# Kernel optimization log

Measured on AMD Instinct MI355X. Metric: run time of the kernel, lower is better.

Reference implementation:

```python
import jax, jax.numpy as jnp
import numpy as np

HID = 512
EMB = 768
TOP_K = 8
LN_EPS = 1e-5
NORM_EPS = 1e-12


def _mlp_ln(x, W1, b1, W2, b2, g, beta):
    # Linear -> ReLU -> Linear -> LayerNorm
    h = jax.nn.relu(x @ W1 + b1)
    h = h @ W2 + b2
    mu = jnp.mean(h, axis=-1, keepdims=True)
    var = jnp.var(h, axis=-1, keepdims=True)
    return (h - mu) * jax.lax.rsqrt(var + LN_EPS) * g + beta


def _l2norm(x):
    n = jnp.linalg.norm(x, axis=-1, keepdims=True)
    return x / jnp.maximum(n, NORM_EPS)


def setup_inputs() -> dict:
    key = jax.random.key(0)
    ks = jax.random.split(key, 12)
    s_in = 1.0 / np.sqrt(EMB)
    s_h = 1.0 / np.sqrt(HID)
    inp = {
        "query_embeddings": jax.random.normal(ks[0], (64, 32, EMB), jnp.float32),
        "doc_embeddings": jax.random.normal(ks[1], (50000, 16, EMB), jnp.float32),
        "qW1": jax.random.normal(ks[2], (EMB, HID), jnp.float32) * s_in,
        "qb1": jnp.zeros((HID,), jnp.float32),
        "qW2": jax.random.normal(ks[3], (HID, HID), jnp.float32) * s_h,
        "qb2": jnp.zeros((HID,), jnp.float32),
        "qg": jnp.ones((HID,), jnp.float32),
        "qbeta": jnp.zeros((HID,), jnp.float32),
        "dW1": jax.random.normal(ks[4], (EMB, HID), jnp.float32) * s_in,
        "db1": jnp.zeros((HID,), jnp.float32),
        "dW2": jax.random.normal(ks[5], (HID, HID), jnp.float32) * s_h,
        "db2": jnp.zeros((HID,), jnp.float32),
        "dg": jnp.ones((HID,), jnp.float32),
        "dbeta": jnp.zeros((HID,), jnp.float32),
        "pW": jax.random.normal(ks[6], (HID, HID), jnp.float32) * s_h,
        "pb": jnp.zeros((HID,), jnp.float32),
        "temperature": jnp.asarray(1.0, jnp.float32),
    }
    return inp


def reference(query_embeddings, doc_embeddings, qW1, qb1, qW2, qb2, qg, qbeta,
              dW1, db1, dW2, db2, dg, dbeta, pW, pb, temperature):
    # Mean-pool over token dims, encode with MLP+LayerNorm
    q_repr = _mlp_ln(query_embeddings.mean(axis=1), qW1, qb1, qW2, qb2, qg, qbeta)  # [B,H]
    d_repr = _mlp_ln(doc_embeddings.mean(axis=1), dW1, db1, dW2, db2, dg, dbeta)    # [N,H]
    q_norm = _l2norm(q_repr @ pW + pb)
    d_norm = _l2norm(d_repr @ pW + pb)
    scores = (q_norm @ d_norm.T) / temperature  # [B,N]
    top_k_scores, top_k_indices = jax.lax.top_k(scores, TOP_K)  # [B,K]
    retrieved_docs = doc_embeddings[top_k_indices]  # [B,K,doc_len,EMB]
    return top_k_scores, retrieved_docs
```

## Files before the change

kernel.cpp:

```cpp
#include <hip/hip_runtime.h>

#define NQ 64
#define ND 50000
#define QTOK 32
#define DTOK 16
#define EMB 768
#define HID 512

typedef short s16x8 __attribute__((ext_vector_type(8)));
typedef float f32x4 __attribute__((ext_vector_type(4)));

__device__ __forceinline__ unsigned short f2bf(float f) {
    union { float f; unsigned u; } x; x.f = f;
    unsigned r = x.u + 0x7fffu + ((x.u >> 16) & 1u);
    return (unsigned short)(r >> 16);
}
__device__ __forceinline__ float bf2f(unsigned short h) {
    union { unsigned u; float f; } x; x.u = ((unsigned)h) << 16;
    return x.f;
}
__device__ __forceinline__ void pack2A(float va, float vb, unsigned& w0, unsigned& w1, unsigned& w2) {
    unsigned ha = f2bf(va); unsigned la = f2bf(va - bf2f((unsigned short)ha));
    unsigned hb = f2bf(vb); unsigned lb = f2bf(vb - bf2f((unsigned short)hb));
    w0 = ha | (la << 16);
    w1 = ha | (hb << 16);
    w2 = lb | (hb << 16);
}
__device__ __forceinline__ void pack2B(float va, float vb, unsigned& w0, unsigned& w1, unsigned& w2) {
    unsigned ha = f2bf(va); unsigned la = f2bf(va - bf2f((unsigned short)ha));
    unsigned hb = f2bf(vb); unsigned lb = f2bf(vb - bf2f((unsigned short)hb));
    w0 = ha | (ha << 16);
    w1 = la | (hb << 16);
    w2 = hb | (lb << 16);
}

__device__ __forceinline__ void gload_lds16(const void* g, void* l) {
    __builtin_amdgcn_global_load_lds(
        (const __attribute__((address_space(1))) void*)g,
        (__attribute__((address_space(3))) void*)l, 16, 0, 0);
}

__global__ void pool_kernel(const float* __restrict__ in, float* __restrict__ out, int T) {
    int r = blockIdx.x;
    int t = threadIdx.x;
    const float4* ip = (const float4*)in + (size_t)r * T * (EMB / 4);
    float4 acc = make_float4(0.f, 0.f, 0.f, 0.f);
    for (int i = 0; i < T; ++i) {
        float4 v = ip[(size_t)i * (EMB / 4) + t];
        acc.x += v.x; acc.y += v.y; acc.z += v.z; acc.w += v.w;
    }
    float s = 1.0f / (float)T;
    acc.x *= s; acc.y *= s; acc.z *= s; acc.w *= s;
    ((float4*)out)[(size_t)r * (EMB / 4) + t] = acc;
}

__global__ void pool_aug(const float* __restrict__ in, ushort* __restrict__ out) {
    int r = blockIdx.x, t = threadIdx.x;
    const float4* ip = (const float4*)in + (size_t)r * DTOK * (EMB / 4) + t;
    float4 a = make_float4(0.f, 0.f, 0.f, 0.f);
    #pragma unroll
    for (int i = 0; i < DTOK; ++i) {
        float4 v = ip[(size_t)i * (EMB / 4)];
        a.x += v.x; a.y += v.y; a.z += v.z; a.w += v.w;
    }
    const float s = 1.0f / (float)DTOK;
    unsigned w0, w1, w2, w3, w4, w5;
    pack2A(a.x * s, a.y * s, w0, w1, w2);
    pack2A(a.z * s, a.w * s, w3, w4, w5);
    uint2* q = (uint2*)(out + (size_t)r * (3 * EMB) + t * 12);
    q[0] = make_uint2(w0, w1); q[1] = make_uint2(w2, w3); q[2] = make_uint2(w4, w5);
}

__global__ void wconv(const float* __restrict__ W, ushort* __restrict__ Wp, int K) {
    int n = blockIdx.x;
    for (int k = threadIdx.x; k < K; k += blockDim.x) {
        float v = W[(size_t)k * HID + n];
        unsigned short hi = f2bf(v);
        unsigned short lo = f2bf(v - bf2f(hi));
        ushort* p = Wp + (size_t)n * 3 * K + 3 * k;
        p[0] = hi; p[1] = hi; p[2] = lo;
    }
}

template <int MODE>
__global__ __launch_bounds__(512) void mfma_gemm2(const ushort* __restrict__ A,
                                                  const ushort* __restrict__ B,
                                                  const float* __restrict__ bias,
                                                  void* __restrict__ out,
                                                  int M, int N_B, int K2, long ldo,
                                                  const float* __restrict__ temp) {
    __shared__ ushort As[128 * 64];
    __shared__ ushort Bs[256 * 64];
    const int bm = blockIdx.x * 128;
    const int bn = blockIdx.y * 256;
    const int tid = threadIdx.x;
    const int lane = tid & 63;
    const int wave = tid >> 6;
    const int wr = wave >> 2;
    const int wc = wave & 3;
    f32x4 acc[4][4] = {};

    for (int k0 = 0; k0 < K2; k0 += 64) {
        #pragma unroll
        for (int c = 0; c < 2; ++c) {
            int row = c * 64 + (tid >> 3);
            int s   = tid & 7;
            int grow = bm + row; if (grow >= M) grow = M - 1;
            int ks = (s ^ (row & 7)) << 3;
            gload_lds16(A + (size_t)grow * K2 + k0 + ks, As + row * 64 + s * 8);
        }
        #pragma unroll
        for (int c = 0; c < 4; ++c) {
            int n = c * 64 + (tid >> 3);
            int s = tid & 7;
            int gn = bn + n; if (gn >= N_B) gn = N_B - 1;
            int ks = (s ^ (n & 7)) << 3;
            gload_lds16(B + (size_t)gn * K2 + k0 + ks, Bs + n * 64 + s * 8);
        }
        __syncthreads();

        #pragma unroll
        for (int kk = 0; kk < 2; ++kk) {
            const int sp = kk * 4 + (lane >> 4);
            s16x8 a[4], b[4];
            #pragma unroll
            for (int i = 0; i < 4; ++i) {
                int r = wr * 64 + i * 16 + (lane & 15);
                a[i] = *(const s16x8*)(As + r * 64 + ((sp ^ (r & 7)) << 3));
            }
            #pragma unroll
            for (int j = 0; j < 4; ++j) {
                int n = wc * 64 + j * 16 + (lane & 15);
                b[j] = *(const s16x8*)(Bs + n * 64 + ((sp ^ (n & 7)) << 3));
            }
            #pragma unroll
            for (int i = 0; i < 4; ++i)
                #pragma unroll
                for (int j = 0; j < 4; ++j)
                    acc[i][j] = __builtin_amdgcn_mfma_f32_16x16x32_bf16(a[i], b[j], acc[i][j], 0, 0, 0);
        }
        __syncthreads();
    }

    float scale = (MODE == 2) ? (1.0f / temp[0]) : 0.0f;
    #pragma unroll
    for (int j = 0; j < 4; ++j) {
        int col = bn + wc * 64 + j * 16 + (lane & 15);
        float bv = (MODE == 2) ? 0.0f : bias[col];
        #pragma unroll
        for (int i = 0; i < 4; ++i) {
            #pragma unroll
            for (int r = 0; r < 4; ++r) {
                int grow = bm + wr * 64 + i * 16 + ((lane >> 4) << 2) + r;
                if (grow >= M) continue;
                float v = acc[i][j][r];
                if (MODE == 0) {
                    ((float*)out)[(size_t)grow * HID + col] = v + bv;
                } else if (MODE == 1) {
                    v = fmaxf(v + bv, 0.0f);
                    unsigned short hi = f2bf(v);
                    unsigned short lo = f2bf(v - bf2f(hi));
                    ushort* op = (ushort*)out + (size_t)grow * (3 * HID) + 3 * col;
                    op[0] = hi; op[1] = lo; op[2] = hi;
                } else {
                    if (col < N_B) ((float*)out)[(size_t)grow * ldo + col] = v * scale;
                }
            }
        }
    }
}

__global__ __launch_bounds__(256) void ln_kernel(float* __restrict__ x,
                                                 const float* __restrict__ g,
                                                 const float* __restrict__ be, int M) {
    int wv = threadIdx.x >> 6, lane = threadIdx.x & 63;
    int row = blockIdx.x * 4 + wv;
    if (row >= M) return;
    float4* p = (float4*)(x + (size_t)row * HID);
    float4 a = p[lane * 2], b = p[lane * 2 + 1];
    float s  = a.x + a.y + a.z + a.w + b.x + b.y + b.z + b.w;
    float sq = a.x*a.x + a.y*a.y + a.z*a.z + a.w*a.w
             + b.x*b.x + b.y*b.y + b.z*b.z + b.w*b.w;
    #pragma unroll
    for (int o = 32; o > 0; o >>= 1) { s += __shfl_xor(s, o); sq += __shfl_xor(sq, o); }
    float mu  = s * (1.0f / HID);
    float var = sq * (1.0f / HID) - mu * mu;
    float r   = rsqrtf(var + 1e-5f);
    const float4* gp = (const float4*)g;
    const float4* bp = (const float4*)be;
    float4 g0 = gp[lane * 2], g1 = gp[lane * 2 + 1];
    float4 b0 = bp[lane * 2], b1 = bp[lane * 2 + 1];
    a.x = (a.x - mu) * r * g0.x + b0.x;  a.y = (a.y - mu) * r * g0.y + b0.y;
    a.z = (a.z - mu) * r * g0.z + b0.z;  a.w = (a.w - mu) * r * g0.w + b0.w;
    b.x = (b.x - mu) * r * g1.x + b1.x;  b.y = (b.y - mu) * r * g1.y + b1.y;
    b.z = (b.z - mu) * r * g1.z + b1.z;  b.w = (b.w - mu) * r * g1.w + b1.w;
    p[lane * 2] = a; p[lane * 2 + 1] = b;
}

__global__ __launch_bounds__(256) void ln_aug(const float* __restrict__ x,
                                              const float* __restrict__ g,
                                              const float* __restrict__ be,
                                              ushort* __restrict__ out, int M) {
    int wv = threadIdx.x >> 6, lane = threadIdx.x & 63;
    int row = blockIdx.x * 4 + wv;
    if (row >= M) return;
    const float4* p = (const float4*)(x + (size_t)row * HID);
    float4 a = p[lane * 2], b = p[lane * 2 + 1];
    float s  = a.x + a.y + a.z + a.w + b.x + b.y + b.z + b.w;
    float sq = a.x*a.x + a.y*a.y + a.z*a.z + a.w*a.w
             + b.x*b.x + b.y*b.y + b.z*b.z + b.w*b.w;
    #pragma unroll
    for (int o = 32; o > 0; o >>= 1) { s += __shfl_xor(s, o); sq += __shfl_xor(sq, o); }
    float mu  = s * (1.0f / HID);
    float var = sq * (1.0f / HID) - mu * mu;
    float r   = rsqrtf(var + 1e-5f);
    const float4* gp = (const float4*)g;
    const float4* bp = (const float4*)be;
    float4 g0 = gp[lane * 2], g1 = gp[lane * 2 + 1];
    float4 b0 = bp[lane * 2], b1 = bp[lane * 2 + 1];
    float v0 = (a.x - mu) * r * g0.x + b0.x, v1 = (a.y - mu) * r * g0.y + b0.y;
    float v2 = (a.z - mu) * r * g0.z + b0.z, v3 = (a.w - mu) * r * g0.w + b0.w;
    float v4 = (b.x - mu) * r * g1.x + b1.x, v5 = (b.y - mu) * r * g1.y + b1.y;
    float v6 = (b.z - mu) * r * g1.z + b1.z, v7 = (b.w - mu) * r * g1.w + b1.w;
    unsigned w[12];
    pack2A(v0, v1, w[0], w[1], w[2]);
    pack2A(v2, v3, w[3], w[4], w[5]);
    pack2A(v4, v5, w[6], w[7], w[8]);
    pack2A(v6, v7, w[9], w[10], w[11]);
    uint4* q = (uint4*)(out + (size_t)row * (3 * HID) + lane * 24);
    q[0] = make_uint4(w[0], w[1], w[2], w[3]);
    q[1] = make_uint4(w[4], w[5], w[6], w[7]);
    q[2] = make_uint4(w[8], w[9], w[10], w[11]);
}

__global__ __launch_bounds__(256) void l2_augB(const float* __restrict__ x,
                                               ushort* __restrict__ out, int M) {
    int wv = threadIdx.x >> 6, lane = threadIdx.x & 63;
    int row = blockIdx.x * 4 + wv;
    if (row >= M) return;
    const float4* p = (const float4*)(x + (size_t)row * HID);
    float4 a = p[lane * 2], b = p[lane * 2 + 1];
    float sq = a.x*a.x + a.y*a.y + a.z*a.z + a.w*a.w
             + b.x*b.x + b.y*b.y + b.z*b.z + b.w*b.w;
    #pragma unroll
    for (int o = 32; o > 0; o >>= 1) sq += __shfl_xor(sq, o);
    float n = sqrtf(sq);
    float r = 1.0f / fmaxf(n, 1e-12f);
    float v0 = a.x*r, v1 = a.y*r, v2 = a.z*r, v3 = a.w*r;
    float v4 = b.x*r, v5 = b.y*r, v6 = b.z*r, v7 = b.w*r;
    unsigned w[12];
    pack2B(v0, v1, w[0], w[1], w[2]);
    pack2B(v2, v3, w[3], w[4], w[5]);
    pack2B(v4, v5, w[6], w[7], w[8]);
    pack2B(v6, v7, w[9], w[10], w[11]);
    uint4* q = (uint4*)(out + (size_t)row * (3 * HID) + lane * 24);
    q[0] = make_uint4(w[0], w[1], w[2], w[3]);
    q[1] = make_uint4(w[4], w[5], w[6], w[7]);
    q[2] = make_uint4(w[8], w[9], w[10], w[11]);
}

__global__ __launch_bounds__(256) void l2_kernel(float* __restrict__ x, int M) {
    int wv = threadIdx.x >> 6, lane = threadIdx.x & 63;
    int row = blockIdx.x * 4 + wv;
    if (row >= M) return;
    float4* p = (float4*)(x + (size_t)row * HID);
    float4 a = p[lane * 2], b = p[lane * 2 + 1];
    float sq = a.x*a.x + a.y*a.y + a.z*a.z + a.w*a.w
             + b.x*b.x + b.y*b.y + b.z*b.z + b.w*b.w;
    #pragma unroll
    for (int o = 32; o > 0; o >>= 1) sq += __shfl_xor(sq, o);
    float n = sqrtf(sq);
    float r = 1.0f / fmaxf(n, 1e-12f);
    a.x *= r; a.y *= r; a.z *= r; a.w *= r;
    b.x *= r; b.y *= r; b.z *= r; b.w *= r;
    p[lane * 2] = a; p[lane * 2 + 1] = b;
}

__global__ __launch_bounds__(256) void fp32_augA(const float* __restrict__ x,
                                                 ushort* __restrict__ out, int M) {
    int wv = threadIdx.x >> 6, lane = threadIdx.x & 63;
    int row = blockIdx.x * 4 + wv;
    if (row >= M) return;
    const float4* p = (const float4*)(x + (size_t)row * HID);
    float4 a = p[lane * 2], b = p[lane * 2 + 1];
    unsigned w[12];
    pack2A(a.x, a.y, w[0], w[1], w[2]);
    pack2A(a.z, a.w, w[3], w[4], w[5]);
    pack2A(b.x, b.y, w[6], w[7], w[8]);
    pack2A(b.z, b.w, w[9], w[10], w[11]);
    uint4* q = (uint4*)(out + (size_t)row * (3 * HID) + lane * 24);
    q[0] = make_uint4(w[0], w[1], w[2], w[3]);
    q[1] = make_uint4(w[4], w[5], w[6], w[7]);
    q[2] = make_uint4(w[8], w[9], w[10], w[11]);
}

template <int RELU>
__global__ __launch_bounds__(256) void gemm_nn(const float* __restrict__ A,
                                               const float* __restrict__ W,
                                               const float* __restrict__ bias,
                                               float* __restrict__ C,
                                               int M, int K, int N) {
    __shared__ float As[16][68];
    __shared__ float Bs[16][64];
    const int bm = blockIdx.x * 64;
    const int bn = blockIdx.y * 64;
    const int tid = threadIdx.x;
    const int tx = tid & 15, ty = tid >> 4;
    float acc[4][4] = {};
    for (int k0 = 0; k0 < K; k0 += 16) {
        {
            int row = tid >> 2;
            int kk  = (tid & 3) << 2;
            int gr  = bm + row;
            float4 v = make_float4(0.f, 0.f, 0.f, 0.f);
            if (gr < M) v = *(const float4*)(A + (size_t)gr * K + k0 + kk);
            As[kk + 0][row] = v.x; As[kk + 1][row] = v.y;
            As[kk + 2][row] = v.z; As[kk + 3][row] = v.w;
        }
        {
            int n  = tid & 63;
            int kb = tid >> 6;
            #pragma unroll
            for (int q = 0; q < 4; ++q) {
                int kr = kb + q * 4;
                Bs[kr][n] = W[(size_t)(k0 + kr) * N + bn + n];
            }
        }
        __syncthreads();
        #pragma unroll
        for (int k = 0; k < 16; ++k) {
            float4 av = *(const float4*)&As[k][ty << 2];
            float4 bv = *(const float4*)&Bs[k][tx << 2];
            float a[4] = {av.x, av.y, av.z, av.w};
            float b[4] = {bv.x, bv.y, bv.z, bv.w};
            #pragma unroll
            for (int i = 0; i < 4; ++i)
                #pragma unroll
                for (int j = 0; j < 4; ++j)
                    acc[i][j] = fmaf(a[i], b[j], acc[i][j]);
        }
        __syncthreads();
    }
    #pragma unroll
    for (int i = 0; i < 4; ++i) {
        int gr = bm + (ty << 2) + i;
        if (gr >= M) continue;
        #pragma unroll
        for (int j = 0; j < 4; ++j) {
            int gc = bn + (tx << 2) + j;
            float v = acc[i][j] + bias[gc];
            if (RELU) v = fmaxf(v, 0.0f);
            C[(size_t)gr * N + gc] = v;
        }
    }
}

__global__ __launch_bounds__(256) void topk_kernel(const float* __restrict__ scores,
                                                   float* __restrict__ out_scores,
                                                   int* __restrict__ out_idx, int N) {
    __shared__ float ls[2048];
    __shared__ int   li[2048];
    const int q   = blockIdx.x;
    const int tid = threadIdx.x;
    const float* row = scores + (size_t)q * N;
    float s[8]; int ix[8];
    #pragma unroll
    for (int i = 0; i < 8; ++i) { s[i] = -1e30f; ix[i] = 0x7fffffff; }
    for (int j = tid; j < N; j += 256) {
        float v = row[j];
        if (v > s[7]) {
            s[7] = v; ix[7] = j;
            #pragma unroll
            for (int t = 7; t > 0; --t) {
                bool sw = (s[t] > s[t-1]) || (s[t] == s[t-1] && ix[t] < ix[t-1]);
                if (sw) {
                    float tv = s[t]; s[t] = s[t-1]; s[t-1] = tv;
                    int   ti = ix[t]; ix[t] = ix[t-1]; ix[t-1] = ti;
                }
            }
        }
    }
    #pragma unroll
    for (int i = 0; i < 8; ++i) { ls[tid * 8 + i] = s[i]; li[tid * 8 + i] = ix[i]; }
    __syncthreads();
    for (int w = 64; w >= 1; w >>= 2) {
        if (tid < w) {
            #pragma unroll
            for (int i = 0; i < 8; ++i) { s[i] = -1e30f; ix[i] = 0x7fffffff; }
            #pragma unroll
            for (int c = 0; c < 32; ++c) {
                float v  = ls[tid * 32 + c];
                int   vi = li[tid * 32 + c];
                bool better = (v > s[7]) || (v == s[7] && vi < ix[7]);
                if (better) {
                    s[7] = v; ix[7] = vi;
                    #pragma unroll
                    for (int t = 7; t > 0; --t) {
                        bool sw = (s[t] > s[t-1]) || (s[t] == s[t-1] && ix[t] < ix[t-1]);
                        if (sw) {
                            float tv = s[t]; s[t] = s[t-1]; s[t-1] = tv;
                            int   ti = ix[t]; ix[t] = ix[t-1]; ix[t-1] = ti;
                        }
                    }
                }
            }
        }
        __syncthreads();
        if (tid < w) {
            #pragma unroll
            for (int i = 0; i < 8; ++i) { ls[tid * 8 + i] = s[i]; li[tid * 8 + i] = ix[i]; }
        }
        __syncthreads();
    }
    if (tid < 8) {
        out_scores[(size_t)q * 8 + tid] = ls[tid];
        out_idx[q * 8 + tid]            = li[tid];
    }
}

__global__ __launch_bounds__(256) void gather_kernel(const float* __restrict__ docs,
                                                     const int* __restrict__ idx,
                                                     float* __restrict__ out) {
    const int b = blockIdx.x;
    const int d = idx[b];
    const float4* src = (const float4*)(docs + (size_t)d * DTOK * EMB);
    float4*       dst = (float4*)(out + (size_t)b * DTOK * EMB);
    for (int i = threadIdx.x; i < DTOK * EMB / 4; i += 256) dst[i] = src[i];
}

extern "C" void kernel_launch(void* const* d_in, const int* in_sizes, int n_in,
                              void* d_out, int out_size, void* d_ws, size_t ws_size,
                              hipStream_t stream) {
    const float* qe   = (const float*)d_in[0];
    const float* de   = (const float*)d_in[1];
    const float* qW1  = (const float*)d_in[2];
    const float* qb1  = (const float*)d_in[3];
    const float* qW2  = (const float*)d_in[4];
    const float* qb2  = (const float*)d_in[5];
    const float* qg   = (const float*)d_in[6];
    const float* qbe  = (const float*)d_in[7];
    const float* dW1  = (const float*)d_in[8];
    const float* db1  = (const float*)d_in[9];
    const float* dW2  = (const float*)d_in[10];
    const float* db2  = (const float*)d_in[11];
    const float* dg   = (const float*)d_in[12];
    const float* dbe  = (const float*)d_in[13];
    const float* pW   = (const float*)d_in[14];
    const float* pb   = (const float*)d_in[15];
    const float* temp = (const float*)d_in[16];

    float* out = (float*)d_out;

    char* w = (char*)d_ws;
    float*  scores = (float*)w;                 w += (size_t)NQ * ND * 4;
    ushort* W1p    = (ushort*)w;                w += (size_t)HID * 3 * EMB * 2;
    ushort* W2p    = (ushort*)w;                w += (size_t)HID * 3 * HID * 2;
    ushort* pWp    = (ushort*)w;                w += (size_t)HID * 3 * HID * 2;
    float*  qpool  = (float*)w;                 w += (size_t)NQ * EMB * 4;
    float*  qh1    = (float*)w;                 w += (size_t)NQ * HID * 4;
    float*  qh2    = (float*)w;                 w += (size_t)NQ * HID * 4;
    float*  qn     = (float*)w;                 w += (size_t)NQ * HID * 4;
    ushort* qaug   = (ushort*)w;                w += (size_t)NQ * 3 * HID * 2;
    int*    tidx   = (int*)w;                   w += 4096;
    ushort* pooled = (ushort*)w;                w += (size_t)ND * 3 * EMB * 2;
    ushort* h1a    = (ushort*)w;                w += (size_t)ND * 3 * HID * 2;
    float*  h2     = (float*)w;                 w += (size_t)ND * HID * 4;
    ushort* lna    = pooled;
    float*  pproj  = h2;
    ushort* Daug   = h1a;

    const int GM = (ND + 127) / 128;

    wconv<<<HID, 256, 0, stream>>>(dW1, W1p, EMB);
    wconv<<<HID, 256, 0, stream>>>(dW2, W2p, HID);
    wconv<<<HID, 256, 0, stream>>>(pW,  pWp, HID);

    pool_kernel<<<NQ, 192, 0, stream>>>(qe, qpool, QTOK);
    gemm_nn<1><<<dim3(1, 8), 256, 0, stream>>>(qpool, qW1, qb1, qh1, NQ, EMB, HID);
    gemm_nn<0><<<dim3(1, 8), 256, 0, stream>>>(qh1, qW2, qb2, qh2, NQ, HID, HID);
    ln_kernel<<<(NQ + 3) / 4, 256, 0, stream>>>(qh2, qg, qbe, NQ);
    gemm_nn<0><<<dim3(1, 8), 256, 0, stream>>>(qh2, pW, pb, qn, NQ, HID, HID);
    l2_kernel<<<(NQ + 3) / 4, 256, 0, stream>>>(qn, NQ);
    fp32_augA<<<(NQ + 3) / 4, 256, 0, stream>>>(qn, qaug, NQ);

    pool_aug<<<ND, 192, 0, stream>>>(de, pooled);
    mfma_gemm2<1><<<dim3(GM, 2), 512, 0, stream>>>(pooled, W1p, db1, h1a, ND, HID, 3 * EMB, 0, nullptr);
    mfma_gemm2<0><<<dim3(GM, 2), 512, 0, stream>>>(h1a, W2p, db2, h2, ND, HID, 3 * HID, 0, nullptr);
    ln_aug<<<(ND + 3) / 4, 256, 0, stream>>>(h2, dg, dbe, lna, ND);
    mfma_gemm2<0><<<dim3(GM, 2), 512, 0, stream>>>(lna, pWp, pb, pproj, ND, HID, 3 * HID, 0, nullptr);
    l2_augB<<<(ND + 3) / 4, 256, 0, stream>>>(pproj, Daug, ND);

    mfma_gemm2<2><<<dim3(1, (ND + 255) / 256), 512, 0, stream>>>(qaug, Daug, nullptr, scores,
                                                                 NQ, ND, 3 * HID, (long)ND, temp);

    topk_kernel<<<NQ, 256, 0, stream>>>(scores, out, tidx, ND);
    gather_kernel<<<NQ * 8, 256, 0, stream>>>(de, tidx, out + NQ * 8);
}
```

Measured before the change: 1.563 ms.

## Fuse LayerNorm and L2 norm into full-row GEMM epilogues, unify query path

Result: slower. 1.594 ms (+2.0%).

```diff
diff --git a/kernel.cpp b/kernel.cpp
--- a/kernel.cpp
+++ b/kernel.cpp
@@ -19,6 +19,16 @@
     union { unsigned u; float f; } x; x.u = ((unsigned)h) << 16;
     return x.f;
 }
+__device__ __forceinline__ void packA1(float v, ushort* p) {
+    unsigned short hi = f2bf(v);
+    unsigned short lo = f2bf(v - bf2f(hi));
+    p[0] = hi; p[1] = lo; p[2] = hi;
+}
+__device__ __forceinline__ void packB1(float v, ushort* p) {
+    unsigned short hi = f2bf(v);
+    unsigned short lo = f2bf(v - bf2f(hi));
+    p[0] = hi; p[1] = hi; p[2] = lo;
+}
 __device__ __forceinline__ void pack2A(float va, float vb, unsigned& w0, unsigned& w1, unsigned& w2) {
     unsigned ha = f2bf(va); unsigned la = f2bf(va - bf2f((unsigned short)ha));
     unsigned hb = f2bf(vb); unsigned lb = f2bf(vb - bf2f((unsigned short)hb));
@@ -26,13 +36,6 @@
     w1 = ha | (hb << 16);
     w2 = lb | (hb << 16);
 }
-__device__ __forceinline__ void pack2B(float va, float vb, unsigned& w0, unsigned& w1, unsigned& w2) {
-    unsigned ha = f2bf(va); unsigned la = f2bf(va - bf2f((unsigned short)ha));
-    unsigned hb = f2bf(vb); unsigned lb = f2bf(vb - bf2f((unsigned short)hb));
-    w0 = ha | (ha << 16);
-    w1 = la | (hb << 16);
-    w2 = hb | (lb << 16);
-}
 
 __device__ __forceinline__ void gload_lds16(const void* g, void* l) {
     __builtin_amdgcn_global_load_lds(
@@ -40,30 +43,15 @@
         (__attribute__((address_space(3))) void*)l, 16, 0, 0);
 }
 
-__global__ void pool_kernel(const float* __restrict__ in, float* __restrict__ out, int T) {
-    int r = blockIdx.x;
-    int t = threadIdx.x;
-    const float4* ip = (const float4*)in + (size_t)r * T * (EMB / 4);
-    float4 acc = make_float4(0.f, 0.f, 0.f, 0.f);
+__global__ void pool_aug(const float* __restrict__ in, ushort* __restrict__ out, int T) {
+    int r = blockIdx.x, t = threadIdx.x;
+    const float4* ip = (const float4*)in + (size_t)r * T * (EMB / 4) + t;
+    float4 a = make_float4(0.f, 0.f, 0.f, 0.f);
     for (int i = 0; i < T; ++i) {
-        float4 v = ip[(size_t)i * (EMB / 4) + t];
-        acc.x += v.x; acc.y += v.y; acc.z += v.z; acc.w += v.w;
-    }
-    float s = 1.0f / (float)T;
-    acc.x *= s; acc.y *= s; acc.z *= s; acc.w *= s;
-    ((float4*)out)[(size_t)r * (EMB / 4) + t] = acc;
-}
-
-__global__ void pool_aug(const float* __restrict__ in, ushort* __restrict__ out) {
-    int r = blockIdx.x, t = threadIdx.x;
-    const float4* ip = (const float4*)in + (size_t)r * DTOK * (EMB / 4) + t;
-    float4 a = make_float4(0.f, 0.f, 0.f, 0.f);
-    #pragma unroll
-    for (int i = 0; i < DTOK; ++i) {
         float4 v = ip[(size_t)i * (EMB / 4)];
         a.x += v.x; a.y += v.y; a.z += v.z; a.w += v.w;
     }
-    const float s = 1.0f / (float)DTOK;
+    const float s = 1.0f / (float)T;
     unsigned w0, w1, w2, w3, w4, w5;
     pack2A(a.x * s, a.y * s, w0, w1, w2);
     pack2A(a.z * s, a.w * s, w3, w4, w5);
@@ -75,47 +63,49 @@
     int n = blockIdx.x;
     for (int k = threadIdx.x; k < K; k += blockDim.x) {
         float v = W[(size_t)k * HID + n];
-        unsigned short hi = f2bf(v);
-        unsigned short lo = f2bf(v - bf2f(hi));
         ushort* p = Wp + (size_t)n * 3 * K + 3 * k;
-        p[0] = hi; p[1] = hi; p[2] = lo;
-    }
-}
-
-template <int MODE>
-__global__ __launch_bounds__(512) void mfma_gemm2(const ushort* __restrict__ A,
-                                                  const ushort* __restrict__ B,
-                                                  const float* __restrict__ bias,
-                                                  void* __restrict__ out,
-                                                  int M, int N_B, int K2, long ldo,
-                                                  const float* __restrict__ temp) {
-    __shared__ ushort As[128 * 64];
-    __shared__ ushort Bs[256 * 64];
-    const int bm = blockIdx.x * 128;
-    const int bn = blockIdx.y * 256;
+        packB1(v, p);
+    }
+}
+
+template <int EPI, int NW>
+__global__ __launch_bounds__(NW * 64) void gemmF(const ushort* __restrict__ A,
+                                                 const ushort* __restrict__ B,
+                                                 const float* __restrict__ bias,
+                                                 const float* __restrict__ gamma,
+                                                 const float* __restrict__ beta,
+                                                 void* __restrict__ out,
+                                                 int M, int N_B, int K2, long ldo,
+                                                 const float* __restrict__ temp) {
+    constexpr int BN = NW * 64;
+    constexpr int NTHR = NW * 64;
+    __shared__ ushort As[64 * 64];
+    __shared__ ushort Bs[BN * 64];
+    __shared__ float red[2][NW][64];
+    __shared__ float mu_s[64], rs_s[64];
+    const int bm = blockIdx.x * 64;
+    const int bn = blockIdx.y * BN;
     const int tid = threadIdx.x;
     const int lane = tid & 63;
-    const int wave = tid >> 6;
-    const int wr = wave >> 2;
-    const int wc = wave & 3;
+    const int wc = tid >> 6;
     f32x4 acc[4][4] = {};
 
     for (int k0 = 0; k0 < K2; k0 += 64) {
         #pragma unroll
-        for (int c = 0; c < 2; ++c) {
-            int row = c * 64 + (tid >> 3);
-            int s   = tid & 7;
-            int grow = bm + row; if (grow >= M) grow = M - 1;
+        for (int c = 0; c < 512 / NTHR; ++c) {
+            int idx = c * NTHR + tid;
+            int row = idx >> 3, s = idx & 7;
+            int gr = bm + row; if (gr >= M) gr = M - 1;
             int ks = (s ^ (row & 7)) << 3;
-            gload_lds16(A + (size_t)grow * K2 + k0 + ks, As + row * 64 + s * 8);
-        }
-        #pragma unroll
-        for (int c = 0; c < 4; ++c) {
-            int n = c * 64 + (tid >> 3);
-            int s = tid & 7;
+            gload_lds16(A + (size_t)gr * K2 + k0 + ks, As + idx * 8);
+        }
+        #pragma unroll
+        for (int c = 0; c < 8; ++c) {
+            int idx = c * NTHR + tid;
+            int n = idx >> 3, s = idx & 7;
             int gn = bn + n; if (gn >= N_B) gn = N_B - 1;
             int ks = (s ^ (n & 7)) << 3;
-            gload_lds16(B + (size_t)gn * K2 + k0 + ks, Bs + n * 64 + s * 8);
+            gload_lds16(B + (size_t)gn * K2 + k0 + ks, Bs + idx * 8);
         }
         __syncthreads();
 
@@ -125,7 +115,7 @@
             s16x8 a[4], b[4];
             #pragma unroll
             for (int i = 0; i < 4; ++i) {
-                int r = wr * 64 + i * 16 + (lane & 15);
+                int r = i * 16 + (lane & 15);
                 a[i] = *(const s16x8*)(As + r * 64 + ((sp ^ (r & 7)) << 3));
             }
             #pragma unroll
@@ -142,217 +132,94 @@
         __syncthreads();
     }
 
-    float scale = (MODE == 2) ? (1.0f / temp[0]) : 0.0f;
-    #pragma unroll
-    for (int j = 0; j < 4; ++j) {
-        int col = bn + wc * 64 + j * 16 + (lane & 15);
-        float bv = (MODE == 2) ? 0.0f : bias[col];
-        #pragma unroll
-        for (int i = 0; i < 4; ++i) {
-            #pragma unroll
-            for (int r = 0; r < 4; ++r) {
-                int grow = bm + wr * 64 + i * 16 + ((lane >> 4) << 2) + r;
-                if (grow >= M) continue;
-                float v = acc[i][j][r];
-                if (MODE == 0) {
-                    ((float*)out)[(size_t)grow * HID + col] = v + bv;
-                } else if (MODE == 1) {
-                    v = fmaxf(v + bv, 0.0f);
-                    unsigned short hi = f2bf(v);
-                    unsigned short lo = f2bf(v - bf2f(hi));
-                    ushort* op = (ushort*)out + (size_t)grow * (3 * HID) + 3 * col;
-                    op[0] = hi; op[1] = lo; op[2] = hi;
-                } else {
-                    if (col < N_B) ((float*)out)[(size_t)grow * ldo + col] = v * scale;
-                }
-            }
-        }
-    }
-}
-
-__global__ __launch_bounds__(256) void ln_kernel(float* __restrict__ x,
-                                                 const float* __restrict__ g,
-                                                 const float* __restrict__ be, int M) {
-    int wv = threadIdx.x >> 6, lane = threadIdx.x & 63;
-    int row = blockIdx.x * 4 + wv;
-    if (row >= M) return;
-    float4* p = (float4*)(x + (size_t)row * HID);
-    float4 a = p[lane * 2], b = p[lane * 2 + 1];
-    float s  = a.x + a.y + a.z + a.w + b.x + b.y + b.z + b.w;
-    float sq = a.x*a.x + a.y*a.y + a.z*a.z + a.w*a.w
-             + b.x*b.x + b.y*b.y + b.z*b.z + b.w*b.w;
-    #pragma unroll
-    for (int o = 32; o > 0; o >>= 1) { s += __shfl_xor(s, o); sq += __shfl_xor(sq, o); }
-    float mu  = s * (1.0f / HID);
-    float var = sq * (1.0f / HID) - mu * mu;
-    float r   = rsqrtf(var + 1e-5f);
-    const float4* gp = (const float4*)g;
-    const float4* bp = (const float4*)be;
-    float4 g0 = gp[lane * 2], g1 = gp[lane * 2 + 1];
-    float4 b0 = bp[lane * 2], b1 = bp[lane * 2 + 1];
-    a.x = (a.x - mu) * r * g0.x + b0.x;  a.y = (a.y - mu) * r * g0.y + b0.y;
-    a.z = (a.z - mu) * r * g0.z + b0.z;  a.w = (a.w - mu) * r * g0.w + b0.w;
-    b.x = (b.x - mu) * r * g1.x + b1.x;  b.y = (b.y - mu) * r * g1.y + b1.y;
-    b.z = (b.z - mu) * r * g1.z + b1.z;  b.w = (b.w - mu) * r * g1.w + b1.w;
-    p[lane * 2] = a; p[lane * 2 + 1] = b;
-}
-
-__global__ __launch_bounds__(256) void ln_aug(const float* __restrict__ x,
-                                              const float* __restrict__ g,
-                                              const float* __restrict__ be,
-                                              ushort* __restrict__ out, int M) {
-    int wv = threadIdx.x >> 6, lane = threadIdx.x & 63;
-    int row = blockIdx.x * 4 + wv;
-    if (row >= M) return;
-    const float4* p = (const float4*)(x + (size_t)row * HID);
-    float4 a = p[lane * 2], b = p[lane * 2 + 1];
-    float s  = a.x + a.y + a.z + a.w + b.x + b.y + b.z + b.w;
-    float sq = a.x*a.x + a.y*a.y + a.z*a.z + a.w*a.w
-             + b.x*b.x + b.y*b.y + b.z*b.z + b.w*b.w;
-    #pragma unroll
-    for (int o = 32; o > 0; o >>= 1) { s += __shfl_xor(s, o); sq += __shfl_xor(sq, o); }
-    float mu  = s * (1.0f / HID);
-    float var = sq * (1.0f / HID) - mu * mu;
-    float r   = rsqrtf(var + 1e-5f);
-    const float4* gp = (const float4*)g;
-    const float4* bp = (const float4*)be;
-    float4 g0 = gp[lane * 2], g1 = gp[lane * 2 + 1];
-    float4 b0 = bp[lane * 2], b1 = bp[lane * 2 + 1];
-    float v0 = (a.x - mu) * r * g0.x + b0.x, v1 = (a.y - mu) * r * g0.y + b0.y;
-    float v2 = (a.z - mu) * r * g0.z + b0.z, v3 = (a.w - mu) * r * g0.w + b0.w;
-    float v4 = (b.x - mu) * r * g1.x + b1.x, v5 = (b.y - mu) * r * g1.y + b1.y;
-    float v6 = (b.z - mu) * r * g1.z + b1.z, v7 = (b.w - mu) * r * g1.w + b1.w;
-    unsigned w[12];
-    pack2A(v0, v1, w[0], w[1], w[2]);
-    pack2A(v2, v3, w[3], w[4], w[5]);
-    pack2A(v4, v5, w[6], w[7], w[8]);
-    pack2A(v6, v7, w[9], w[10], w[11]);
-    uint4* q = (uint4*)(out + (size_t)row * (3 * HID) + lane * 24);
-    q[0] = make_uint4(w[0], w[1], w[2], w[3]);
-    q[1] = make_uint4(w[4], w[5], w[6], w[7]);
-    q[2] = make_uint4(w[8], w[9], w[10], w[11]);
-}
-
-__global__ __launch_bounds__(256) void l2_augB(const float* __restrict__ x,
-                                               ushort* __restrict__ out, int M) {
-    int wv = threadIdx.x >> 6, lane = threadIdx.x & 63;
-    int row = blockIdx.x * 4 + wv;
-    if (row >= M) return;
-    const float4* p = (const float4*)(x + (size_t)row * HID);
-    float4 a = p[lane * 2], b = p[lane * 2 + 1];
-    float sq = a.x*a.x + a.y*a.y + a.z*a.z + a.w*a.w
-             + b.x*b.x + b.y*b.y + b.z*b.z + b.w*b.w;
-    #pragma unroll
-    for (int o = 32; o > 0; o >>= 1) sq += __shfl_xor(sq, o);
-    float n = sqrtf(sq);
-    float r = 1.0f / fmaxf(n, 1e-12f);
-    float v0 = a.x*r, v1 = a.y*r, v2 = a.z*r, v3 = a.w*r;
-    float v4 = b.x*r, v5 = b.y*r, v6 = b.z*r, v7 = b.w*r;
-    unsigned w[12];
-    pack2B(v0, v1, w[0], w[1], w[2]);
-    pack2B(v2, v3, w[3], w[4], w[5]);
-    pack2B(v4, v5, w[6], w[7], w[8]);
-    pack2B(v6, v7, w[9], w[10], w[11]);
-    uint4* q = (uint4*)(out + (size_t)row * (3 * HID) + lane * 24);
-    q[0] = make_uint4(w[0], w[1], w[2], w[3]);
-    q[1] = make_uint4(w[4], w[5], w[6], w[7]);
-    q[2] = make_uint4(w[8], w[9], w[10], w[11]);
-}
-
-__global__ __launch_bounds__(256) void l2_kernel(float* __restrict__ x, int M) {
-    int wv = threadIdx.x >> 6, lane = threadIdx.x & 63;
-    int row = blockIdx.x * 4 + wv;
-    if (row >= M) return;
-    float4* p = (float4*)(x + (size_t)row * HID);
-    float4 a = p[lane * 2], b = p[lane * 2 + 1];
-    float sq = a.x*a.x + a.y*a.y + a.z*a.z + a.w*a.w
-             + b.x*b.x + b.y*b.y + b.z*b.z + b.w*b.w;
-    #pragma unroll
-    for (int o = 32; o > 0; o >>= 1) sq += __shfl_xor(sq, o);
-    float n = sqrtf(sq);
-    float r = 1.0f / fmaxf(n, 1e-12f);
-    a.x *= r; a.y *= r; a.z *= r; a.w *= r;
-    b.x *= r; b.y *= r; b.z *= r; b.w *= r;
-    p[lane * 2] = a; p[lane * 2 + 1] = b;
-}
-
-__global__ __launch_bounds__(256) void fp32_augA(const float* __restrict__ x,
-                                                 ushort* __restrict__ out, int M) {
-    int wv = threadIdx.x >> 6, lane = threadIdx.x & 63;
-    int row = blockIdx.x * 4 + wv;
-    if (row >= M) return;
-    const float4* p = (const float4*)(x + (size_t)row * HID);
-    float4 a = p[lane * 2], b = p[lane * 2 + 1];
-    unsigned w[12];
-    pack2A(a.x, a.y, w[0], w[1], w[2]);
-    pack2A(a.z, a.w, w[3], w[4], w[5]);
-    pack2A(b.x, b.y, w[6], w[7], w[8]);
-    pack2A(b.z, b.w, w[9], w[10], w[11]);
-    uint4* q = (uint4*)(out + (size_t)row * (3 * HID) + lane * 24);
-    q[0] = make_uint4(w[0], w[1], w[2], w[3]);
-    q[1] = make_uint4(w[4], w[5], w[6], w[7]);
-    q[2] = make_uint4(w[8], w[9], w[10], w[11]);
-}
-
-template <int RELU>
-__global__ __launch_bounds__(256) void gemm_nn(const float* __restrict__ A,
-                                               const float* __restrict__ W,
-                                               const float* __restrict__ bias,
-                                               float* __restrict__ C,
-                                               int M, int K, int N) {
-    __shared__ float As[16][68];
-    __shared__ float Bs[16][64];
-    const int bm = blockIdx.x * 64;
-    const int bn = blockIdx.y * 64;
-    const int tid = threadIdx.x;
-    const int tx = tid & 15, ty = tid >> 4;
-    float acc[4][4] = {};
-    for (int k0 = 0; k0 < K; k0 += 16) {
-        {
-            int row = tid >> 2;
-            int kk  = (tid & 3) << 2;
-            int gr  = bm + row;
-            float4 v = make_float4(0.f, 0.f, 0.f, 0.f);
-            if (gr < M) v = *(const float4*)(A + (size_t)gr * K + k0 + kk);
-            As[kk + 0][row] = v.x; As[kk + 1][row] = v.y;
-            As[kk + 2][row] = v.z; As[kk + 3][row] = v.w;
-        }
-        {
-            int n  = tid & 63;
-            int kb = tid >> 6;
-            #pragma unroll
-            for (int q = 0; q < 4; ++q) {
-                int kr = kb + q * 4;
-                Bs[kr][n] = W[(size_t)(k0 + kr) * N + bn + n];
-            }
-        }
-        __syncthreads();
-        #pragma unroll
-        for (int k = 0; k < 16; ++k) {
-            float4 av = *(const float4*)&As[k][ty << 2];
-            float4 bv = *(const float4*)&Bs[k][tx << 2];
-            float a[4] = {av.x, av.y, av.z, av.w};
-            float b[4] = {bv.x, bv.y, bv.z, bv.w};
+    if (EPI == 4) {
+        float invT = 1.0f / temp[0];
+        #pragma unroll
+        for (int j = 0; j < 4; ++j) {
+            int gcol = bn + wc * 64 + j * 16 + (lane & 15);
             #pragma unroll
             for (int i = 0; i < 4; ++i)
                 #pragma unroll
-                for (int j = 0; j < 4; ++j)
-                    acc[i][j] = fmaf(a[i], b[j], acc[i][j]);
-        }
-        __syncthreads();
-    }
+                for (int r = 0; r < 4; ++r) {
+                    int grow = bm + i * 16 + ((lane >> 4) << 2) + r;
+                    if (grow < M && gcol < N_B)
+                        ((float*)out)[(size_t)grow * ldo + gcol] = acc[i][j][r] * invT;
+                }
+        }
+        return;
+    }
+
+    float bv[4];
     #pragma unroll
-    for (int i = 0; i < 4; ++i) {
-        int gr = bm + (ty << 2) + i;
-        if (gr >= M) continue;
+    for (int j = 0; j < 4; ++j) bv[j] = bias[wc * 64 + j * 16 + (lane & 15)];
+
+    if (EPI == 1 || EPI == 2 || EPI == 3) {
+        #pragma unroll
+        for (int i = 0; i < 4; ++i)
+            #pragma unroll
+            for (int r = 0; r < 4; ++r) {
+                float ps = 0.f, pq = 0.f;
+                #pragma unroll
+                for (int j = 0; j < 4; ++j) {
+                    float v = acc[i][j][r] + bv[j];
+                    ps += v; pq += v * v;
+                }
+                #pragma unroll
+                for (int o = 1; o < 16; o <<= 1) {
+                    ps += __shfl_xor(ps, o);
+                    pq += __shfl_xor(pq, o);
+                }
+                if ((lane & 15) == 0) {
+                    int rl = i * 16 + ((lane >> 4) << 2) + r;
+                    red[0][wc][rl] = ps;
+                    red[1][wc][rl] = pq;
+                }
+            }
+        __syncthreads();
+        if (tid < 64) {
+            float s = 0.f, q = 0.f;
+            #pragma unroll
+            for (int w = 0; w < NW; ++w) { s += red[0][w][tid]; q += red[1][w][tid]; }
+            if (EPI == 1) {
+                float mu = s * (1.0f / 512.0f);
+                float var = q * (1.0f / 512.0f) - mu * mu;
+                mu_s[tid] = mu;
+                rs_s[tid] = rsqrtf(var + 1e-5f);
+            } else {
+                mu_s[tid] = 0.0f;
+                rs_s[tid] = 1.0f / fmaxf(sqrtf(q), 1e-12f);
+            }
+        }
+        __syncthreads();
+    }
+
+    float gl[4], bt[4];
+    if (EPI == 1) {
         #pragma unroll
         for (int j = 0; j < 4; ++j) {
-            int gc = bn + (tx << 2) + j;
-            float v = acc[i][j] + bias[gc];
-            if (RELU) v = fmaxf(v, 0.0f);
-            C[(size_t)gr * N + gc] = v;
-        }
-    }
+            int c = wc * 64 + j * 16 + (lane & 15);
+            gl[j] = gamma[c]; bt[j] = beta[c];
+        }
+    }
+
+    #pragma unroll
+    for (int i = 0; i < 4; ++i)
+        #pragma unroll
+        for (int r = 0; r < 4; ++r) {
+            int rl = i * 16 + ((lane >> 4) << 2) + r;
+            int grow = bm + rl;
+            if (grow >= M) continue;
+            #pragma unroll
+            for (int j = 0; j < 4; ++j) {
+                int col = wc * 64 + j * 16 + (lane & 15);
+                float v = acc[i][j][r] + bv[j];
+                if (EPI == 0) v = fmaxf(v, 0.0f);
+                else if (EPI == 1) v = (v - mu_s[rl]) * rs_s[rl] * gl[j] + bt[j];
+                else v = v * rs_s[rl];
+                ushort* op = (ushort*)out + (size_t)grow * (3 * HID) + 3 * col;
+                if (EPI == 3) packB1(v, op); else packA1(v, op);
+            }
+        }
 }
 
 __global__ __launch_bounds__(256) void topk_kernel(const float* __restrict__ scores,
@@ -456,42 +323,44 @@
     ushort* W1p    = (ushort*)w;                w += (size_t)HID * 3 * EMB * 2;
     ushort* W2p    = (ushort*)w;                w += (size_t)HID * 3 * HID * 2;
     ushort* pWp    = (ushort*)w;                w += (size_t)HID * 3 * HID * 2;
-    float*  qpool  = (float*)w;                 w += (size_t)NQ * EMB * 4;
-    float*  qh1    = (float*)w;                 w += (size_t)NQ * HID * 4;
-    float*  qh2    = (float*)w;                 w += (size_t)NQ * HID * 4;
-    float*  qn     = (float*)w;                 w += (size_t)NQ * HID * 4;
+    ushort* QW1p   = (ushort*)w;                w += (size_t)HID * 3 * EMB * 2;
+    ushort* QW2p   = (ushort*)w;                w += (size_t)HID * 3 * HID * 2;
+    ushort* qpool  = (ushort*)w;                w += (size_t)NQ * 3 * EMB * 2;
+    ushort* qh1a   = (ushort*)w;                w += (size_t)NQ * 3 * HID * 2;
+    ushort* qlna   = (ushort*)w;                w += (size_t)NQ * 3 * HID * 2;
     ushort* qaug   = (ushort*)w;                w += (size_t)NQ * 3 * HID * 2;
     int*    tidx   = (int*)w;                   w += 4096;
     ushort* pooled = (ushort*)w;                w += (size_t)ND * 3 * EMB * 2;
     ushort* h1a    = (ushort*)w;                w += (size_t)ND * 3 * HID * 2;
-    float*  h2     = (float*)w;                 w += (size_t)ND * HID * 4;
     ushort* lna    = pooled;
-    float*  pproj  = h2;
     ushort* Daug   = h1a;
 
-    const int GM = (ND + 127) / 128;
+    const int GMD = (ND + 63) / 64;
 
     wconv<<<HID, 256, 0, stream>>>(dW1, W1p, EMB);
     wconv<<<HID, 256, 0, stream>>>(dW2, W2p, HID);
     wconv<<<HID, 256, 0, stream>>>(pW,  pWp, HID);
-
-    pool_kernel<<<NQ, 192, 0, stream>>>(qe, qpool, QTOK);
-    gemm_nn<1><<<dim3(1, 8), 256, 0, stream>>>(qpool, qW1, qb1, qh1, NQ, EMB, HID);
-    gemm_nn<0><<<dim3(1, 8), 256, 0, stream>>>(qh1, qW2, qb2, qh2, NQ, HID, HID);
-    ln_kernel<<<(NQ + 3) / 4, 256, 0, stream>>>(qh2, qg, qbe, NQ);
-    gemm_nn<0><<<dim3(1, 8), 256, 0, stream>>>(qh2, pW, pb, qn, NQ, HID, HID);
-    l2_kernel<<<(NQ + 3) / 4, 256, 0, stream>>>(qn, NQ);
-    fp32_augA<<<(NQ + 3) / 4, 256, 0, stream>>>(qn, qaug, NQ);
-
-    pool_aug<<<ND, 192, 0, stream>>>(de, pooled);
-    mfma_gemm2<1><<<dim3(GM, 2), 512, 0, stream>>>(pooled, W1p, db1, h1a, ND, HID, 3 * EMB, 0, nullptr);
-    mfma_gemm2<0><<<dim3(GM, 2), 512, 0, stream>>>(h1a, W2p, db2, h2, ND, HID, 3 * HID, 0, nullptr);
-    ln_aug<<<(ND + 3) / 4, 256, 0, stream>>>(h2, dg, dbe, lna, ND);
-    mfma_gemm2<0><<<dim3(GM, 2), 512, 0, stream>>>(lna, pWp, pb, pproj, ND, HID, 3 * HID, 0, nullptr);
-    l2_augB<<<(ND + 3) / 4, 256, 0, stream>>>(pproj, Daug, ND);
-
-    mfma_gemm2<2><<<dim3(1, (ND + 255) / 256), 512, 0, stream>>>(qaug, Daug, nullptr, scores,
-                                                                 NQ, ND, 3 * HID, (long)ND, temp);
+    wconv<<<HID, 256, 0, stream>>>(qW1, QW1p, EMB);
+    wconv<<<HID, 256, 0, stream>>>(qW2, QW2p, HID);
+
+    pool_aug<<<NQ, 192, 0, stream>>>(qe, qpool, QTOK);
+    gemmF<0, 8><<<dim3(1, 1), 512, 0, stream>>>(qpool, QW1p, qb1, nullptr, nullptr, qh1a,
+                                                NQ, HID, 3 * EMB, 0, nullptr);
+    gemmF<1, 8><<<dim3(1, 1), 512, 0, stream>>>(qh1a, QW2p, qb2, qg, qbe, qlna,
+                                                NQ, HID, 3 * HID, 0, nullptr);
+    gemmF<2, 8><<<dim3(1, 1), 512, 0, stream>>>(qlna, pWp, pb, nullptr, nullptr, qaug,
+                                                NQ, HID, 3 * HID, 0, nullptr);
+
+    pool_aug<<<ND, 192, 0, stream>>>(de, pooled, DTOK);
+    gemmF<0, 8><<<dim3(GMD, 1), 512, 0, stream>>>(pooled, W1p, db1, nullptr, nullptr, h1a,
+                                                  ND, HID, 3 * EMB, 0, nullptr);
+    gemmF<1, 8><<<dim3(GMD, 1), 512, 0, stream>>>(h1a, W2p, db2, dg, dbe, lna,
+                                                  ND, HID, 3 * HID, 0, nullptr);
+    gemmF<3, 8><<<dim3(GMD, 1), 512, 0, stream>>>(lna, pWp, pb, nullptr, nullptr, Daug,
+                                                  ND, HID, 3 * HID, 0, nullptr);
+
+    gemmF<4, 4><<<dim3(1, (ND + 255) / 256), 256, 0, stream>>>(qaug, Daug, nullptr, nullptr, nullptr,
+                                                               scores, NQ, ND, 3 * HID, (long)ND, temp);
 
     topk_kernel<<<NQ, 256, 0, stream>>>(scores, out, tidx, ND);
     gather_kernel<<<NQ * 8, 256, 0, stream>>>(de, tidx, out + NQ * 8);
```

## Enlarge doc-encoder GEMM tiles to 256x256 with XCD-aware block remapping

Applied to the files above, without the earlier changes.

New measurement: 1.696 ms. 1.09x slower.

```diff
diff --git a/kernel.cpp b/kernel.cpp
--- a/kernel.cpp
+++ b/kernel.cpp
@@ -83,12 +83,93 @@
 }
 
 template <int MODE>
-__global__ __launch_bounds__(512) void mfma_gemm2(const ushort* __restrict__ A,
+__global__ __launch_bounds__(512) void mfma_gemm3(const ushort* __restrict__ A,
                                                   const ushort* __restrict__ B,
                                                   const float* __restrict__ bias,
                                                   void* __restrict__ out,
-                                                  int M, int N_B, int K2, long ldo,
-                                                  const float* __restrict__ temp) {
+                                                  int M, int K2) {
+    __shared__ ushort As[256 * 64];
+    __shared__ ushort Bs[256 * 64];
+    const int d  = blockIdx.x;
+    const int pr = (d & 7) * 49 + (d >> 3);
+    const int bm = (pr >> 1) * 256;
+    const int bn = (pr & 1) * 256;
+    const int tid = threadIdx.x;
+    const int lane = tid & 63;
+    const int wave = tid >> 6;
+    const int wr = wave >> 2;
+    const int wc = wave & 3;
+    f32x4 acc[8][4] = {};
+
+    for (int k0 = 0; k0 < K2; k0 += 64) {
+        #pragma unroll
+        for (int c = 0; c < 4; ++c) {
+            int idx = c * 512 + tid;
+            int row = idx >> 3, s = idx & 7;
+            int gr = bm + row; if (gr >= M) gr = M - 1;
+            int ks = (s ^ (row & 7)) << 3;
+            gload_lds16(A + (size_t)gr * K2 + k0 + ks, As + idx * 8);
+        }
+        #pragma unroll
+        for (int c = 0; c < 4; ++c) {
+            int idx = c * 512 + tid;
+            int n = idx >> 3, s = idx & 7;
+            int ks = (s ^ (n & 7)) << 3;
+            gload_lds16(B + (size_t)(bn + n) * K2 + k0 + ks, Bs + idx * 8);
+        }
+        __syncthreads();
+
+        #pragma unroll
+        for (int kk = 0; kk < 2; ++kk) {
+            const int sp = kk * 4 + (lane >> 4);
+            s16x8 b[4];
+            #pragma unroll
+            for (int j = 0; j < 4; ++j) {
+                int n = wc * 64 + j * 16 + (lane & 15);
+                b[j] = *(const s16x8*)(Bs + n * 64 + ((sp ^ (n & 7)) << 3));
+            }
+            #pragma unroll
+            for (int i = 0; i < 8; ++i) {
+                int r = wr * 128 + i * 16 + (lane & 15);
+                s16x8 a = *(const s16x8*)(As + r * 64 + ((sp ^ (r & 7)) << 3));
+                #pragma unroll
+                for (int j = 0; j < 4; ++j)
+                    acc[i][j] = __builtin_amdgcn_mfma_f32_16x16x32_bf16(a, b[j], acc[i][j], 0, 0, 0);
+            }
+        }
+        __syncthreads();
+    }
+
+    #pragma unroll
+    for (int j = 0; j < 4; ++j) {
+        int col = bn + wc * 64 + j * 16 + (lane & 15);
+        float bv = bias[col];
+        #pragma unroll
+        for (int i = 0; i < 8; ++i) {
+            #pragma unroll
+            for (int r = 0; r < 4; ++r) {
+                int grow = bm + wr * 128 + i * 16 + ((lane >> 4) << 2) + r;
+                if (grow >= M) continue;
+                float v = acc[i][j][r] + bv;
+                if (MODE == 1) {
+                    v = fmaxf(v, 0.0f);
+                    unsigned short hi = f2bf(v);
+                    unsigned short lo = f2bf(v - bf2f(hi));
+                    ushort* op = (ushort*)out + (size_t)grow * (3 * HID) + 3 * col;
+                    op[0] = hi; op[1] = lo; op[2] = hi;
+                } else {
+                    ((float*)out)[(size_t)grow * HID + col] = v;
+                }
+            }
+        }
+    }
+}
+
+__global__ __launch_bounds__(512) void mfma_scores(const ushort* __restrict__ A,
+                                                   const ushort* __restrict__ B,
+                                                   float* __restrict__ out,
+                                                   int M, int N_B, int K2, long ldo,
+                                                   const float* __restrict__ temp) {
     __shared__ ushort As[128 * 64];
     __shared__ ushort Bs[256 * 64];
     const int bm = blockIdx.x * 128;
@@ -103,19 +184,19 @@
     for (int k0 = 0; k0 < K2; k0 += 64) {
         #pragma unroll
         for (int c = 0; c < 2; ++c) {
-            int row = c * 64 + (tid >> 3);
-            int s   = tid & 7;
-            int grow = bm + row; if (grow >= M) grow = M - 1;
+            int idx = c * 512 + tid;
+            int row = idx >> 3, s = idx & 7;
+            int gr = bm + row; if (gr >= M) gr = M - 1;
             int ks = (s ^ (row & 7)) << 3;
-            gload_lds16(A + (size_t)grow * K2 + k0 + ks, As + row * 64 + s * 8);
+            gload_lds16(A + (size_t)gr * K2 + k0 + ks, As + idx * 8);
         }
         #pragma unroll
         for (int c = 0; c < 4; ++c) {
-            int n = c * 64 + (tid >> 3);
-            int s = tid & 7;
+            int idx = c * 512 + tid;
+            int n = idx >> 3, s = idx & 7;
             int gn = bn + n; if (gn >= N_B) gn = N_B - 1;
             int ks = (s ^ (n & 7)) << 3;
-            gload_lds16(B + (size_t)gn * K2 + k0 + ks, Bs + n * 64 + s * 8);
+            gload_lds16(B + (size_t)gn * K2 + k0 + ks, Bs + idx * 8);
         }
         __syncthreads();
 
@@ -142,31 +223,18 @@
         __syncthreads();
     }
 
-    float scale = (MODE == 2) ? (1.0f / temp[0]) : 0.0f;
+    float invT = 1.0f / temp[0];
     #pragma unroll
     for (int j = 0; j < 4; ++j) {
-        int col = bn + wc * 64 + j * 16 + (lane & 15);
-        float bv = (MODE == 2) ? 0.0f : bias[col];
-        #pragma unroll
-        for (int i = 0; i < 4; ++i) {
+        int gcol = bn + wc * 64 + j * 16 + (lane & 15);
+        #pragma unroll
+        for (int i = 0; i < 4; ++i)
             #pragma unroll
             for (int r = 0; r < 4; ++r) {
                 int grow = bm + wr * 64 + i * 16 + ((lane >> 4) << 2) + r;
-                if (grow >= M) continue;
-                float v = acc[i][j][r];
-                if (MODE == 0) {
-                    ((float*)out)[(size_t)grow * HID + col] = v + bv;
-                } else if (MODE == 1) {
-                    v = fmaxf(v + bv, 0.0f);
-                    unsigned short hi = f2bf(v);
-                    unsigned short lo = f2bf(v - bf2f(hi));
-                    ushort* op = (ushort*)out + (size_t)grow * (3 * HID) + 3 * col;
-                    op[0] = hi; op[1] = lo; op[2] = hi;
-                } else {
-                    if (col < N_B) ((float*)out)[(size_t)grow * ldo + col] = v * scale;
-                }
-            }
-        }
+                if (grow < M && gcol < N_B)
+                    out[(size_t)grow * ldo + gcol] = acc[i][j][r] * invT;
+            }
     }
 }
 
@@ -469,8 +537,6 @@
     float*  pproj  = h2;
     ushort* Daug   = h1a;
 
-    const int GM = (ND + 127) / 128;
-
     wconv<<<HID, 256, 0, stream>>>(dW1, W1p, EMB);
     wconv<<<HID, 256, 0, stream>>>(dW2, W2p, HID);
     wconv<<<HID, 256, 0, stream>>>(pW,  pWp, HID);
@@ -484,14 +550,14 @@
     fp32_augA<<<(NQ + 3) / 4, 256, 0, stream>>>(qn, qaug, NQ);
 
     pool_aug<<<ND, 192, 0, stream>>>(de, pooled);
-    mfma_gemm2<1><<<dim3(GM, 2), 512, 0, stream>>>(pooled, W1p, db1, h1a, ND, HID, 3 * EMB, 0, nullptr);
-    mfma_gemm2<0><<<dim3(GM, 2), 512, 0, stream>>>(h1a, W2p, db2, h2, ND, HID, 3 * HID, 0, nullptr);
+    mfma_gemm3<1><<<392, 512, 0, stream>>>(pooled, W1p, db1, h1a, ND, 3 * EMB);
+    mfma_gemm3<0><<<392, 512, 0, stream>>>(h1a, W2p, db2, h2, ND, 3 * HID);
     ln_aug<<<(ND + 3) / 4, 256, 0, stream>>>(h2, dg, dbe, lna, ND);
-    mfma_gemm2<0><<<dim3(GM, 2), 512, 0, stream>>>(lna, pWp, pb, pproj, ND, HID, 3 * HID, 0, nullptr);
+    mfma_gemm3<0><<<392, 512, 0, stream>>>(lna, pWp, pb, pproj, ND, 3 * HID);
     l2_augB<<<(ND + 3) / 4, 256, 0, stream>>>(pproj, Daug, ND);
 
-    mfma_gemm2<2><<<dim3(1, (ND + 255) / 256), 512, 0, stream>>>(qaug, Daug, nullptr, scores,
-                                                                 NQ, ND, 3 * HID, (long)ND, temp);
+    mfma_scores<<<dim3(1, (ND + 255) / 256), 512, 0, stream>>>(qaug, Daug, scores,
+                                                               NQ, ND, 3 * HID, (long)ND, temp);
 
     topk_kernel<<<NQ, 256, 0, stream>>>(scores, out, tidx, ND);
     gather_kernel<<<NQ * 8, 256, 0, stream>>>(de, tidx, out + NQ * 8);
```
